# Kernel tuning notes

Measured on AMD Instinct MI355X. Metric: run time of the kernel, lower is better.

Reference implementation:

```python
import jax, jax.numpy as jnp
import numpy as np
import math

HID = 512
HEADS = 8
DK = HID // HEADS
B, S, T = 8, 4096, 512


def setup_inputs() -> dict:
    key = jax.random.key(0)
    ks = jax.random.split(key, 12)
    scale = 0.02
    inp = {
        "inputs": jax.random.normal(ks[0], (B, S, HID), dtype=jnp.float32),
        "targets": jax.random.normal(ks[1], (B, T, HID), dtype=jnp.float32),
        "mask": jnp.ones((B, S), dtype=bool),
        "Wq": jax.random.normal(ks[2], (HID, HID), dtype=jnp.float32) * scale,
        "bq": jnp.zeros((HID,), dtype=jnp.float32),
        "Wk": jax.random.normal(ks[3], (HID, HID), dtype=jnp.float32) * scale,
        "bk": jnp.zeros((HID,), dtype=jnp.float32),
        "Wv": jax.random.normal(ks[4], (HID, HID), dtype=jnp.float32) * scale,
        "bv": jnp.zeros((HID,), dtype=jnp.float32),
        "Wo": jax.random.normal(ks[5], (HID, HID), dtype=jnp.float32) * scale,
        "bo": jnp.zeros((HID,), dtype=jnp.float32),
    }
    return inp


def reference(inputs, targets, mask, Wq, bq, Wk, bk, Wv, bv, Wo, bo):
    # PoolingFunction(method='multihead-attention'), dropout=0 (identity),
    # hidden_size == output_size so mapping_function is identity.
    b, t, h = targets.shape
    s = inputs.shape[1]
    Q = (targets @ Wq.T + bq).reshape(b, t, HEADS, DK)
    K = (inputs @ Wk.T + bk).reshape(b, s, HEADS, DK)
    V = (inputs @ Wv.T + bv).reshape(b, s, HEADS, DK)
    # scores: b x heads x tgt x seq (same math as (Q*K).sum(-1)/sqrt(d_k))
    e = jnp.einsum('bthd,bshd->bhts', Q, K) / math.sqrt(DK)
    neg = (1.0 - mask.astype(jnp.float32)) * -1e20  # b x s
    e = e + neg[:, None, None, :]
    a = jax.nn.softmax(e, axis=-1)  # softmax over seq dim
    ctx = jnp.einsum('bhts,bshd->bthd', a, V).reshape(b, t, h)
    return ctx @ Wo.T + bo
```

## Files before the change

kernel.cpp:

```cpp
#include <hip/hip_runtime.h>
#include <hip/hip_bf16.h>
#include <cstdint>
#include <cstddef>

#define HIDN   512
#define NHEADS 8
#define BATCH  8
#define SLEN   4096
#define TLEN   512
#define SSPLIT 4
#define SCHUNK (SLEN / SSPLIT)
#define SCL2   0.18033688f

typedef __attribute__((ext_vector_type(8))) short   bf16x8;
typedef __attribute__((ext_vector_type(4))) float   f32x4;
typedef unsigned short u16;
typedef unsigned int   u32;

__device__ __forceinline__ u32 pkbf(float a, float b) {
    __hip_bfloat162 h = __float22bfloat162_rn(float2{a, b});
    union { __hip_bfloat162 h; u32 u; } un; un.h = h; return un.u;
}
__device__ __forceinline__ u32 pk2(float a, float b) {
    union { float f; u32 u; } ua, ub; ua.f = a; ub.f = b;
    return __builtin_amdgcn_perm(ub.u + 0x8000u, ua.u + 0x8000u, 0x07060302u);
}
__device__ __forceinline__ u32 cvtpk(float a, float b) {
    u32 r;
    asm("v_cvt_pk_bf16_f32 %0, %1, %2" : "=v"(r) : "v"(a), "v"(b));
    return r;
}
__device__ __forceinline__ void gload_lds16(const u16* g, u16* l) {
    __builtin_amdgcn_global_load_lds(
        (const __attribute__((address_space(1))) u32*)g,
        (__attribute__((address_space(3))) u32*)l, 16, 0, 0);
}

__global__ __launch_bounds__(256) void cvt_all(
    const float* __restrict__ X, const float* __restrict__ Tg,
    const float* __restrict__ Wq, const float* __restrict__ Wk,
    const float* __restrict__ Wv, const float* __restrict__ Wo,
    const int* __restrict__ mask,
    u16* __restrict__ Xc, u16* __restrict__ Tc, u16* __restrict__ Wc,
    float* __restrict__ negf)
{
    int i4 = blockIdx.x * 256 + threadIdx.x;
    if (i4 >= 4980736) {
        int off = i4 - 4980736;
        int4 mv = ((const int4*)mask)[off];
        float4 nv;
        nv.x = mv.x ? 0.f : -1e30f; nv.y = mv.y ? 0.f : -1e30f;
        nv.z = mv.z ? 0.f : -1e30f; nv.w = mv.w ? 0.f : -1e30f;
        ((float4*)negf)[off] = nv;
        return;
    }
    const float* s; u16* d; long off;
    if (i4 < 4194304)      { s = X;  d = Xc; off = i4; }
    else if (i4 < 4718592) { s = Tg; d = Tc; off = i4 - 4194304; }
    else {
        int wi = i4 - 4718592; int widx = wi >> 16;
        s = (widx == 0) ? Wq : (widx == 1) ? Wk : (widx == 2) ? Wv : Wo;
        d = Wc + widx * 262144; off = wi & 65535;
    }
    float4 v = *(const float4*)(s + off * 4);
    uint2 o; o.x = pkbf(v.x, v.y); o.y = pkbf(v.z, v.w);
    *(uint2*)(d + off * 4) = o;
}

template<int MODE, int SEQ>
__global__ __launch_bounds__(256)
void gemm_bf16(const u16* __restrict__ A, const u16* __restrict__ Bw,
               const float* __restrict__ bias, void* __restrict__ Yv)
{
    __shared__ u16 As[128 * 32];
    __shared__ u16 Bs[128 * 32];
    const int tid = threadIdx.x;
    const int lane = tid & 63, w = tid >> 6;
    const int m = lane & 15, qd = lane >> 4;
    const int wm = w >> 1, wn = w & 1;
    const int m0 = blockIdx.y * 128, n0 = blockIdx.x * 128;

    f32x4 acc[4][4];
#pragma unroll
    for (int i = 0; i < 4; ++i)
#pragma unroll
        for (int j = 0; j < 4; ++j) acc[i][j] = (f32x4){0.f, 0.f, 0.f, 0.f};

    for (int k0 = 0; k0 < HIDN; k0 += 32) {
#pragma unroll
        for (int r = 0; r < 2; ++r) {
            const int f = tid + r * 256;
            const int row = f >> 2, c8 = (f & 3) * 8;
            const int fb = f & ~63;
            gload_lds16(A  + (size_t)(m0 + row) * HIDN + k0 + c8, As + fb * 8);
            gload_lds16(Bw + (size_t)(n0 + row) * HIDN + k0 + c8, Bs + fb * 8);
        }
        __syncthreads();
        bf16x8 af[4], bf[4];
#pragma unroll
        for (int t = 0; t < 4; ++t) {
            af[t] = *(bf16x8*)&As[(64 * wm + 16 * t + m) * 32 + 8 * qd];
            bf[t] = *(bf16x8*)&Bs[(64 * wn + 16 * t + m) * 32 + 8 * qd];
        }
#pragma unroll
        for (int ti = 0; ti < 4; ++ti)
#pragma unroll
            for (int tj = 0; tj < 4; ++tj)
                acc[ti][tj] = __builtin_amdgcn_mfma_f32_16x16x32_bf16(
                    af[ti], bf[tj], acc[ti][tj], 0, 0, 0);
        __syncthreads();
    }

#pragma unroll
    for (int ti = 0; ti < 4; ++ti) {
        const int gr0 = m0 + 64 * wm + 16 * ti + 4 * qd;
#pragma unroll
        for (int tj = 0; tj < 4; ++tj) {
            const int gcol = n0 + 64 * wn + 16 * tj + m;
            const float bv = bias[gcol];
            if (MODE == 0) {
                float* Y = (float*)Yv;
#pragma unroll
                for (int i = 0; i < 4; ++i)
                    Y[(size_t)(gr0 + i) * HIDN + gcol] = acc[ti][tj][i] + bv;
            } else {
                u16* Y = (u16*)Yv;
                const int b = gr0 / SEQ, h = gcol >> 6, d = gcol & 63;
                const int r = gr0 & (SEQ - 1);
                uint2 o;
                o.x = pkbf(acc[ti][tj][0] + bv, acc[ti][tj][1] + bv);
                o.y = pkbf(acc[ti][tj][2] + bv, acc[ti][tj][3] + bv);
                *(uint2*)&Y[(((size_t)(b * 8 + h)) * 64 + d) * SEQ + r] = o;
            }
        }
    }
}

template<int SEQ>
__global__ __launch_bounds__(256)
void gemm_wxT(const u16* __restrict__ Wm, const u16* __restrict__ X,
              const float* __restrict__ bias, u16* __restrict__ Y)
{
    __shared__ u16 As[128 * 32];
    __shared__ u16 Bs[128 * 32];
    const int tid = threadIdx.x;
    const int lane = tid & 63, w = tid >> 6;
    const int m = lane & 15, qd = lane >> 4;
    const int wm = w >> 1, wn = w & 1;
    const int m0 = blockIdx.y * 128, n0 = blockIdx.x * 128;

    f32x4 acc[4][4];
#pragma unroll
    for (int i = 0; i < 4; ++i)
#pragma unroll
        for (int j = 0; j < 4; ++j) acc[i][j] = (f32x4){0.f, 0.f, 0.f, 0.f};

    for (int k0 = 0; k0 < HIDN; k0 += 32) {
#pragma unroll
        for (int r = 0; r < 2; ++r) {
            const int f = tid + r * 256;
            const int row = f >> 2, c8 = (f & 3) * 8;
            const int fb = f & ~63;
            gload_lds16(Wm + (size_t)(m0 + row) * HIDN + k0 + c8, As + fb * 8);
            gload_lds16(X  + (size_t)(n0 + row) * HIDN + k0 + c8, Bs + fb * 8);
        }
        __syncthreads();
        bf16x8 af[4], bf[4];
#pragma unroll
        for (int t = 0; t < 4; ++t) {
            af[t] = *(bf16x8*)&As[(64 * wm + 16 * t + m) * 32 + 8 * qd];
            bf[t] = *(bf16x8*)&Bs[(64 * wn + 16 * t + m) * 32 + 8 * qd];
        }
#pragma unroll
        for (int ti = 0; ti < 4; ++ti)
#pragma unroll
            for (int tj = 0; tj < 4; ++tj)
                acc[ti][tj] = __builtin_amdgcn_mfma_f32_16x16x32_bf16(
                    af[ti], bf[tj], acc[ti][tj], 0, 0, 0);
        __syncthreads();
    }

#pragma unroll
    for (int ti = 0; ti < 4; ++ti) {
        const int o = m0 + 64 * wm + 16 * ti + 4 * qd;
        const float4 bv = *(const float4*)&bias[o];
        const int h = o >> 6, d0 = o & 63;
#pragma unroll
        for (int tj = 0; tj < 4; ++tj) {
            const int n = n0 + 64 * wn + 16 * tj + m;
            const int b = n / SEQ, r = n & (SEQ - 1);
            uint2 pk;
            pk.x = pkbf(acc[ti][tj][0] + bv.x, acc[ti][tj][1] + bv.y);
            pk.y = pkbf(acc[ti][tj][2] + bv.z, acc[ti][tj][3] + bv.w);
            *(uint2*)&Y[(((size_t)(b * 8 + h)) * SEQ + r) * 64 + d0] = pk;
        }
    }
}

__global__ __launch_bounds__(256, 2)
void attn_part(const u16* __restrict__ Q, const u16* __restrict__ K,
               const u16* __restrict__ Vt, const float* __restrict__ negf,
               float* __restrict__ Opart, float* __restrict__ lpart)
{
    __shared__ char Psh[32768];
    const int tid = threadIdx.x;
    const int lane = tid & 63, w = tid >> 6;
    const int m = lane & 15, qd = lane >> 4;
    const int ti = blockIdx.x, si = blockIdx.y, bh = blockIdx.z;
    const int b = bh >> 3;

    const u16* Qp = Q + ((size_t)bh * TLEN + ti * 256) * 64;
    const u16* Kp = K + (size_t)bh * SLEN * 64;
    const u16* Vp = Vt + (size_t)bh * 64 * SLEN;
    const float* np = negf + (size_t)b * SLEN;

    const int wb = w * 8192 + m * 128;
    int waddr[4], ra0[2], ra1[2];
#pragma unroll
    for (int st = 0; st < 4; ++st) waddr[st] = wb + (((4 * st + qd) ^ m) << 3);
#pragma unroll
    for (int ks = 0; ks < 2; ++ks) {
        const int u0 = 8 * ks + 2 * qd;
        ra0[ks] = wb + (((u0) ^ m) << 3);
        ra1[ks] = wb + (((u0 + 1) ^ m) << 3);
    }

    bf16x8 qf[4][2];
#pragma unroll
    for (int ts = 0; ts < 4; ++ts)
#pragma unroll
        for (int kh = 0; kh < 2; ++kh)
            qf[ts][kh] = *(const bf16x8*)(Qp + (64 * w + 16 * ts + m) * 64 +
                                          32 * kh + 8 * qd);

    f32x4 O[4][4];
#pragma unroll
    for (int ts = 0; ts < 4; ++ts)
#pragma unroll
        for (int dt = 0; dt < 4; ++dt) O[ts][dt] = (f32x4){0.f, 0.f, 0.f, 0.f};
    float lr[4] = {0.f, 0.f, 0.f, 0.f};

    const int s_beg = si * SCHUNK;
    const u16* kp = Kp + (size_t)(s_beg + m) * 64 + 8 * qd;
    const u16* vp0 = Vp + (size_t)m * SLEN + s_beg + 8 * qd;
    const u16* vp1 = vp0 + (size_t)16 * SLEN;
    const u16* vp2 = vp0 + (size_t)32 * SLEN;
    const u16* vp3 = vp0 + (size_t)48 * SLEN;
    const float* npp = np + s_beg + 4 * qd;

#define LOADK(kf, ng) do {                                                   \
        kf[0][0] = *(const bf16x8*)(kp + 0);                                 \
        kf[0][1] = *(const bf16x8*)(kp + 32);                                \
        kf[1][0] = *(const bf16x8*)(kp + 1024);                              \
        kf[1][1] = *(const bf16x8*)(kp + 1056);                              \
        kf[2][0] = *(const bf16x8*)(kp + 2048);                              \
        kf[2][1] = *(const bf16x8*)(kp + 2080);                              \
        kf[3][0] = *(const bf16x8*)(kp + 3072);                              \
        kf[3][1] = *(const bf16x8*)(kp + 3104);                              \
        ng[0] = *(const float4*)(npp + 0);                                   \
        ng[1] = *(const float4*)(npp + 16);                                  \
        ng[2] = *(const float4*)(npp + 32);                                  \
        ng[3] = *(const float4*)(npp + 48);                                  \
        kp += 4096; npp += 64; } while (0)

#define LOADV(vf) do {                                                       \
        vf[0][0] = *(const bf16x8*)(vp0 + 0);                                \
        vf[0][1] = *(const bf16x8*)(vp0 + 32);                               \
        vf[1][0] = *(const bf16x8*)(vp1 + 0);                                \
        vf[1][1] = *(const bf16x8*)(vp1 + 32);                               \
        vf[2][0] = *(const bf16x8*)(vp2 + 0);                                \
        vf[2][1] = *(const bf16x8*)(vp2 + 32);                               \
        vf[3][0] = *(const bf16x8*)(vp3 + 0);                                \
        vf[3][1] = *(const bf16x8*)(vp3 + 32);                               \
        vp0 += 64; vp1 += 64; vp2 += 64; vp3 += 64; } while (0)

#define QKPHASE(kf, ng) do {                                                 \
        _Pragma("unroll")                                                    \
        for (int ts = 0; ts < 4; ++ts) {                                     \
            f32x4 S[4];                                                      \
            _Pragma("unroll")                                                \
            for (int st = 0; st < 4; ++st) {                                 \
                f32x4 cc = (f32x4){0.f, 0.f, 0.f, 0.f};                      \
                cc = __builtin_amdgcn_mfma_f32_16x16x32_bf16(                \
                         kf[st][0], qf[ts][0], cc, 0, 0, 0);                 \
                cc = __builtin_amdgcn_mfma_f32_16x16x32_bf16(                \
                         kf[st][1], qf[ts][1], cc, 0, 0, 0);                 \
                S[st] = cc;                                                  \
            }                                                                \
            float ls = 0.f;                                                  \
            _Pragma("unroll")                                                \
            for (int st = 0; st < 4; ++st) {                                 \
                const float p0 = exp2f(fmaf(S[st][0], SCL2, ng[st].x));      \
                const float p1 = exp2f(fmaf(S[st][1], SCL2, ng[st].y));      \
                const float p2 = exp2f(fmaf(S[st][2], SCL2, ng[st].z));      \
                const float p3 = exp2f(fmaf(S[st][3], SCL2, ng[st].w));      \
                ls += (p0 + p1) + (p2 + p3);                                 \
                *(uint2*)&Psh[waddr[st] + ts * 2048] =                       \
                    make_uint2(cvtpk(p0, p1), cvtpk(p2, p3));                \
            }                                                                \
            lr[ts] += ls;                                                    \
        } } while (0)

#define PVPHASE(vf) do {                                                     \
        __builtin_amdgcn_s_setprio(1);                                       \
        _Pragma("unroll")                                                    \
        for (int ts = 0; ts < 4; ++ts) {                                     \
            _Pragma("unroll")                                                \
            for (int ks = 0; ks < 2; ++ks) {                                 \
                const uint2 r0 = *(uint2*)&Psh[ra0[ks] + ts * 2048];         \
                const uint2 r1 = *(uint2*)&Psh[ra1[ks] + ts * 2048];         \
                union { uint4 u; bf16x8 v; } bu;                             \
                bu.u = make_uint4(r0.x, r0.y, r1.x, r1.y);                   \
                O[ts][0] = __builtin_amdgcn_mfma_f32_16x16x32_bf16(          \
                               vf[0][ks], bu.v, O[ts][0], 0, 0, 0);          \
                O[ts][1] = __builtin_amdgcn_mfma_f32_16x16x32_bf16(          \
                               vf[1][ks], bu.v, O[ts][1], 0, 0, 0);          \
                O[ts][2] = __builtin_amdgcn_mfma_f32_16x16x32_bf16(          \
                               vf[2][ks], bu.v, O[ts][2], 0, 0, 0);          \
                O[ts][3] = __builtin_amdgcn_mfma_f32_16x16x32_bf16(          \
                               vf[3][ks], bu.v, O[ts][3], 0, 0, 0);          \
            }                                                                \
        }                                                                    \
        __builtin_amdgcn_s_setprio(0); } while (0)

    bf16x8 kf[4][2], vf[4][2];
    float4 ng[4];

    LOADK(kf, ng);
#pragma unroll 1
    for (int c = 0; c < (SCHUNK / 64) - 1; ++c) {
        LOADV(vf);
        QKPHASE(kf, ng);
        LOADK(kf, ng);
        PVPHASE(vf);
    }
    LOADV(vf);
    QKPHASE(kf, ng);
    PVPHASE(vf);

#undef LOADK
#undef LOADV
#undef QKPHASE
#undef PVPHASE

#pragma unroll
    for (int ts = 0; ts < 4; ++ts) {
        float l = lr[ts];
        l += __shfl_xor(l, 16, 64);
        l += __shfl_xor(l, 32, 64);
        const int t = ti * 256 + 64 * w + 16 * ts + m;
        float* Ob = Opart + (((size_t)(si * 64 + bh)) * 512 + t) * 64;
#pragma unroll
        for (int dt = 0; dt < 4; ++dt)
            *(f32x4*)&Ob[16 * dt + 4 * qd] = O[ts][dt];
        if (qd == 0)
            lpart[((size_t)(si * 64 + bh)) * 512 + t] = l;
    }
}

__global__ __launch_bounds__(256)
void attn_combine(const float* __restrict__ Opart, const float* __restrict__ lpart,
                  u16* __restrict__ ctx)
{
    const int gid = blockIdx.x * 256 + threadIdx.x;
    const int d4 = gid & 15, t = (gid >> 4) & 511, bh = gid >> 13;
    const int b = bh >> 3, h = bh & 7;
    float4 o = {0.f, 0.f, 0.f, 0.f}; float l = 0.f;
#pragma unroll
    for (int si = 0; si < SSPLIT; ++si) {
        const size_t base = ((size_t)(si * 64 + bh)) * 512 + t;
        l += lpart[base];
        const float4 v = *(const float4*)(Opart + base * 64 + d4 * 4);
        o.x += v.x; o.y += v.y; o.z += v.z; o.w += v.w;
    }
    const float r = 1.f / l;
    uint2 pk; pk.x = pkbf(o.x * r, o.y * r); pk.y = pkbf(o.z * r, o.w * r);
    *(uint2*)&ctx[((size_t)(b * 512 + t)) * 512 + h * 64 + d4 * 4] = pk;
}

extern "C" void kernel_launch(void* const* d_in, const int* in_sizes, int n_in,
                              void* d_out, int out_size, void* d_ws, size_t ws_size,
                              hipStream_t stream)
{
    const float* inputs  = (const float*)d_in[0];
    const float* targets = (const float*)d_in[1];
    const int*   mask    = (const int*)d_in[2];
    const float* Wq = (const float*)d_in[3];
    const float* bq = (const float*)d_in[4];
    const float* Wk = (const float*)d_in[5];
    const float* bk = (const float*)d_in[6];
    const float* Wv = (const float*)d_in[7];
    const float* bv = (const float*)d_in[8];
    const float* Wo = (const float*)d_in[9];
    const float* bo = (const float*)d_in[10];

    char* ws = (char*)d_ws;
    u16*   Xc    = (u16*)(ws);
    u16*   Tc    = (u16*)(ws + 33554432);
    u16*   Wc    = (u16*)(ws + 37748736);
    float* negf  = (float*)(ws + 39845888);
    u16*   Qws   = (u16*)(ws + 39976960);
    u16*   Kws   = (u16*)(ws + 44171264);
    u16*   Vtws  = (u16*)(ws + 77725696);
    u16*   Cws   = (u16*)(ws + 111280128);
    float* Opart = (float*)(ws + 115474432);
    float* lpart = (float*)(ws + 149028864);

    cvt_all<<<19488, 256, 0, stream>>>(inputs, targets, Wq, Wk, Wv, Wo, mask,
                                       Xc, Tc, Wc, negf);

    gemm_wxT<TLEN><<<dim3(32, 4),  256, 0, stream>>>(Wc,          Tc, bq, Qws);
    gemm_wxT<SLEN><<<dim3(256, 4), 256, 0, stream>>>(Wc + 262144, Xc, bk, Kws);
    gemm_bf16<2, SLEN><<<dim3(4, 256), 256, 0, stream>>>(Xc, Wc + 524288, bv, Vtws);

    attn_part<<<dim3(2, SSPLIT, 64), 256, 0, stream>>>(Qws, Kws, Vtws, negf,
                                                       Opart, lpart);
    attn_combine<<<2048, 256, 0, stream>>>(Opart, lpart, Cws);

    gemm_bf16<0, TLEN><<<dim3(4, 32), 256, 0, stream>>>(Cws, Wc + 786432, bo,
                                                        (float*)d_out);
}
```

Before: 294.2 us.

## Stage K/V tiles through double-buffered LDS with async global-to-LDS loads

The attention kernel no longer has each wave load K and V fragments straight from global memory into registers. All four waves now share one copy of each 64-row K/V chunk, loaded into double-buffered LDS with global_load_lds and read back through a swizzled layout. The mask offsets for the whole split are also preloaded into LDS. This cuts redundant global traffic, since each wave previously fetched the same K/V, but it adds two barriers per chunk and about 33KB more LDS, which may lower occupancy.

```diff
diff --git a/kernel.cpp b/kernel.cpp
--- a/kernel.cpp
+++ b/kernel.cpp
@@ -20,10 +20,6 @@
 __device__ __forceinline__ u32 pkbf(float a, float b) {
     __hip_bfloat162 h = __float22bfloat162_rn(float2{a, b});
     union { __hip_bfloat162 h; u32 u; } un; un.h = h; return un.u;
-}
-__device__ __forceinline__ u32 pk2(float a, float b) {
-    union { float f; u32 u; } ua, ub; ua.f = a; ub.f = b;
-    return __builtin_amdgcn_perm(ub.u + 0x8000u, ua.u + 0x8000u, 0x07060302u);
 }
 __device__ __forceinline__ u32 cvtpk(float a, float b) {
     u32 r;
@@ -203,6 +199,8 @@
                float* __restrict__ Opart, float* __restrict__ lpart)
 {
     __shared__ char Psh[32768];
+    __shared__ u16  KVl[2][8192];
+    __shared__ float Ngl[1024];
     const int tid = threadIdx.x;
     const int lane = tid & 63, w = tid >> 6;
     const int m = lane & 15, qd = lane >> 4;
@@ -213,6 +211,25 @@
     const u16* Kp = K + (size_t)bh * SLEN * 64;
     const u16* Vp = Vt + (size_t)bh * 64 * SLEN;
     const float* np = negf + (size_t)b * SLEN;
+    const int s_beg = si * SCHUNK;
+
+    const int sr = tid >> 3;
+    const int sg = ((tid & 7) ^ (sr & 7)) * 8;
+    const u16* kgb = Kp + (size_t)s_beg * 64 + sr * 64 + sg;
+    const u16* vgb = Vp + s_beg + (size_t)sr * SLEN + sg;
+    u16* kd = &KVl[0][0]    + tid * 8;
+    u16* vd = &KVl[0][4096] + tid * 8;
+
+#define STAGE(cc, bb) do {                                                   \
+        const u16* kg_ = kgb + (size_t)(cc) * 4096;                          \
+        const u16* vg_ = vgb + (cc) * 64;                                    \
+        u16* kd_ = kd + (bb) * 8192;                                         \
+        u16* vd_ = vd + (bb) * 8192;                                         \
+        gload_lds16(kg_,                     kd_);                           \
+        gload_lds16(kg_ + 32 * 64,           kd_ + 2048);                    \
+        gload_lds16(vg_,                     vd_);                           \
+        gload_lds16(vg_ + (size_t)32 * SLEN, vd_ + 2048);                    \
+    } while (0)
 
     const int wb = w * 8192 + m * 128;
     int waddr[4], ra0[2], ra1[2];
@@ -224,6 +241,8 @@
         ra0[ks] = wb + (((u0) ^ m) << 3);
         ra1[ks] = wb + (((u0 + 1) ^ m) << 3);
     }
+    const int x0 = ((qd    ) ^ (m & 7)) * 8;
+    const int x1 = ((4 + qd) ^ (m & 7)) * 8;
 
     bf16x8 qf[4][2];
 #pragma unroll
@@ -240,52 +259,30 @@
         for (int dt = 0; dt < 4; ++dt) O[ts][dt] = (f32x4){0.f, 0.f, 0.f, 0.f};
     float lr[4] = {0.f, 0.f, 0.f, 0.f};
 
-    const int s_beg = si * SCHUNK;
-    const u16* kp = Kp + (size_t)(s_beg + m) * 64 + 8 * qd;
-    const u16* vp0 = Vp + (size_t)m * SLEN + s_beg + 8 * qd;
-    const u16* vp1 = vp0 + (size_t)16 * SLEN;
-    const u16* vp2 = vp0 + (size_t)32 * SLEN;
-    const u16* vp3 = vp0 + (size_t)48 * SLEN;
-    const float* npp = np + s_beg + 4 * qd;
-
-#define LOADK(kf, ng) do {                                                   \
-        kf[0][0] = *(const bf16x8*)(kp + 0);                                 \
-        kf[0][1] = *(const bf16x8*)(kp + 32);                                \
-        kf[1][0] = *(const bf16x8*)(kp + 1024);                              \
-        kf[1][1] = *(const bf16x8*)(kp + 1056);                              \
-        kf[2][0] = *(const bf16x8*)(kp + 2048);                              \
-        kf[2][1] = *(const bf16x8*)(kp + 2080);                              \
-        kf[3][0] = *(const bf16x8*)(kp + 3072);                              \
-        kf[3][1] = *(const bf16x8*)(kp + 3104);                              \
-        ng[0] = *(const float4*)(npp + 0);                                   \
-        ng[1] = *(const float4*)(npp + 16);                                  \
-        ng[2] = *(const float4*)(npp + 32);                                  \
-        ng[3] = *(const float4*)(npp + 48);                                  \
-        kp += 4096; npp += 64; } while (0)
-
-#define LOADV(vf) do {                                                       \
-        vf[0][0] = *(const bf16x8*)(vp0 + 0);                                \
-        vf[0][1] = *(const bf16x8*)(vp0 + 32);                               \
-        vf[1][0] = *(const bf16x8*)(vp1 + 0);                                \
-        vf[1][1] = *(const bf16x8*)(vp1 + 32);                               \
-        vf[2][0] = *(const bf16x8*)(vp2 + 0);                                \
-        vf[2][1] = *(const bf16x8*)(vp2 + 32);                               \
-        vf[3][0] = *(const bf16x8*)(vp3 + 0);                                \
-        vf[3][1] = *(const bf16x8*)(vp3 + 32);                               \
-        vp0 += 64; vp1 += 64; vp2 += 64; vp3 += 64; } while (0)
-
-#define QKPHASE(kf, ng) do {                                                 \
+#define CHUNK(cc) do {                                                       \
+        const u16* Kl = &KVl[(cc) & 1][0];                                   \
+        const u16* Vl = &KVl[(cc) & 1][4096];                                \
+        bf16x8 kf[4][2];                                                     \
+        _Pragma("unroll")                                                    \
+        for (int st = 0; st < 4; ++st) {                                     \
+            kf[st][0] = *(const bf16x8*)&Kl[st * 1024 + m * 64 + x0];        \
+            kf[st][1] = *(const bf16x8*)&Kl[st * 1024 + m * 64 + x1];        \
+        }                                                                    \
+        float4 ng[4];                                                        \
+        _Pragma("unroll")                                                    \
+        for (int st = 0; st < 4; ++st)                                       \
+            ng[st] = *(const float4*)&Ngl[((cc) << 6) + (st << 4) + (qd << 2)]; \
         _Pragma("unroll")                                                    \
         for (int ts = 0; ts < 4; ++ts) {                                     \
             f32x4 S[4];                                                      \
             _Pragma("unroll")                                                \
             for (int st = 0; st < 4; ++st) {                                 \
-                f32x4 cc = (f32x4){0.f, 0.f, 0.f, 0.f};                      \
-                cc = __builtin_amdgcn_mfma_f32_16x16x32_bf16(                \
-                         kf[st][0], qf[ts][0], cc, 0, 0, 0);                 \
-                cc = __builtin_amdgcn_mfma_f32_16x16x32_bf16(                \
-                         kf[st][1], qf[ts][1], cc, 0, 0, 0);                 \
-                S[st] = cc;                                                  \
+                f32x4 cc2 = (f32x4){0.f, 0.f, 0.f, 0.f};                     \
+                cc2 = __builtin_amdgcn_mfma_f32_16x16x32_bf16(               \
+                          kf[st][0], qf[ts][0], cc2, 0, 0, 0);               \
+                cc2 = __builtin_amdgcn_mfma_f32_16x16x32_bf16(               \
+                          kf[st][1], qf[ts][1], cc2, 0, 0, 0);               \
+                S[st] = cc2;                                                 \
             }                                                                \
             float ls = 0.f;                                                  \
             _Pragma("unroll")                                                \
@@ -299,9 +296,13 @@
                     make_uint2(cvtpk(p0, p1), cvtpk(p2, p3));                \
             }                                                                \
             lr[ts] += ls;                                                    \
-        } } while (0)
-
-#define PVPHASE(vf) do {                                                     \
+        }                                                                    \
+        bf16x8 vf[4][2];                                                     \
+        _Pragma("unroll")                                                    \
+        for (int dt = 0; dt < 4; ++dt) {                                     \
+            vf[dt][0] = *(const bf16x8*)&Vl[dt * 1024 + m * 64 + x0];        \
+            vf[dt][1] = *(const bf16x8*)&Vl[dt * 1024 + m * 64 + x1];        \
+        }                                                                    \
         __builtin_amdgcn_s_setprio(1);                                       \
         _Pragma("unroll")                                                    \
         for (int ts = 0; ts < 4; ++ts) {                                     \
@@ -321,27 +322,29 @@
                                vf[3][ks], bu.v, O[ts][3], 0, 0, 0);          \
             }                                                                \
         }                                                                    \
-        __builtin_amdgcn_s_setprio(0); } while (0)
-
-    bf16x8 kf[4][2], vf[4][2];
-    float4 ng[4];
-
-    LOADK(kf, ng);
+        __builtin_amdgcn_s_setprio(0);                                       \
+    } while (0)
+
+    STAGE(0, 0);
+    gload_lds16((const u16*)(np + s_beg) + (size_t)tid * 8,
+                ((u16*)Ngl) + tid * 8);
 #pragma unroll 1
     for (int c = 0; c < (SCHUNK / 64) - 1; ++c) {
-        LOADV(vf);
-        QKPHASE(kf, ng);
-        LOADK(kf, ng);
-        PVPHASE(vf);
-    }
-    LOADV(vf);
-    QKPHASE(kf, ng);
-    PVPHASE(vf);
-
-#undef LOADK
-#undef LOADV
-#undef QKPHASE
-#undef PVPHASE
+        STAGE(c + 1, (c + 1) & 1);
+        asm volatile("s_waitcnt vmcnt(4)" ::: "memory");
+        __builtin_amdgcn_s_barrier();
+        __builtin_amdgcn_sched_barrier(0);
+        CHUNK(c);
+        __builtin_amdgcn_s_barrier();
+        __builtin_amdgcn_sched_barrier(0);
+    }
+    asm volatile("s_waitcnt vmcnt(0)" ::: "memory");
+    __builtin_amdgcn_s_barrier();
+    __builtin_amdgcn_sched_barrier(0);
+    CHUNK((SCHUNK / 64) - 1);
+
+#undef STAGE
+#undef CHUNK
 
 #pragma unroll
     for (int ts = 0; ts < 4; ++ts) {
```

Result: no change. 289.4 us (-1.6%).
